# Kernel optimization log

Hardware: AMD Instinct MI355X
Metric: run time of the kernel (lower is better)

The kernel has to match this reference:

```python
import jax, jax.numpy as jnp
import numpy as np

S, H = 8192, 2048

def setup_inputs() -> dict:
    key = jax.random.key(0)
    k1, k2, k3 = jax.random.split(key, 3)
    hidden = jax.random.normal(k1, (1, H), dtype=jnp.float32)
    encoder_outputs = jax.random.normal(k2, (S, 1, H), dtype=jnp.float32)
    W = jax.random.normal(k3, (H, H), dtype=jnp.float32) * (1.0 / np.sqrt(H))
    b = jnp.zeros((H,), dtype=jnp.float32)
    return {"hidden": hidden, "encoder_outputs": encoder_outputs, "W": W, "b": b}

def reference(hidden, encoder_outputs, W, b):
    # hidden: [1, H] -> [H]; encoder_outputs: [S, 1, H] -> [S, H]
    h = hidden[0]                      # [H]
    enc = encoder_outputs[:, 0, :]     # [S, H]
    # method='general': energy_i = h . (W @ enc_i + b)
    proj = jnp.einsum('sh,kh->sk', enc, W) + b   # [S, H] (Linear: x @ W.T + b)
    energies = proj @ h                          # [S]
    attn = jax.nn.softmax(energies, axis=0)      # softmax over seq dim
    return attn[None, None, :]                   # [1, 1, S]
```

## Files before the change

### kernel.cpp

```cpp
#include <hip/hip_runtime.h>


#define Hdim 2048
#define Sdim 8192
#define PCHUNKS 128
#define PROWS 16

__global__ void k1_partial(const float* __restrict__ W, const float* __restrict__ hid,
                           float* __restrict__ part) {
    int t = threadIdx.x;
    int colBase = blockIdx.x * 1024 + t * 4;
    int k0 = blockIdx.y * PROWS;
    float4 acc = {0.f, 0.f, 0.f, 0.f};
#pragma unroll
    for (int i = 0; i < PROWS; ++i) {
        int k = k0 + i;
        float hk = hid[k];
        float4 w = *reinterpret_cast<const float4*>(W + (size_t)k * Hdim + colBase);
        acc.x += w.x * hk;
        acc.y += w.y * hk;
        acc.z += w.z * hk;
        acc.w += w.w * hk;
    }
    *reinterpret_cast<float4*>(part + (size_t)blockIdx.y * Hdim + colBase) = acc;
}

__global__ void k1b_reduce(const float* __restrict__ part, float* __restrict__ v) {
    __shared__ float red[256];
    int t = threadIdx.x;
    int col = blockIdx.x * 64 + (t & 63);
    int j0 = (t >> 6) * 32;
    float s = 0.f;
#pragma unroll
    for (int j = 0; j < 32; ++j) s += part[(size_t)(j0 + j) * Hdim + col];
    red[t] = s;
    __syncthreads();
    if (t < 64) v[col] = red[t] + red[64 + t] + red[128 + t] + red[192 + t];
}

__global__ void k2_energies(const float* __restrict__ enc, const float* __restrict__ v,
                            float* __restrict__ e) {
    int t = threadIdx.x;
    int lane = t & 63;
    int s = blockIdx.x * 4 + (t >> 6);
    const float* row = enc + (size_t)s * Hdim;
    float acc = 0.f;
#pragma unroll
    for (int i = 0; i < 8; ++i) {
        int idx = i * 256 + lane * 4;
        float4 a = *reinterpret_cast<const float4*>(row + idx);
        float4 w = *reinterpret_cast<const float4*>(v + idx);
        acc += a.x * w.x + a.y * w.y + a.z * w.z + a.w * w.w;
    }
#pragma unroll
    for (int off = 32; off > 0; off >>= 1) acc += __shfl_xor(acc, off, 64);
    if (lane == 0) e[s] = acc;
}

__global__ void k3_softmax(const float* __restrict__ e, float* __restrict__ out) {
    __shared__ float red[16];
    __shared__ float bcast;
    int t = threadIdx.x;
    int lane = t & 63, wid = t >> 6;
    float4 a = *reinterpret_cast<const float4*>(e + t * 8);
    float4 bq = *reinterpret_cast<const float4*>(e + t * 8 + 4);
    float vals[8] = {a.x, a.y, a.z, a.w, bq.x, bq.y, bq.z, bq.w};
    float m = vals[0];
#pragma unroll
    for (int i = 1; i < 8; ++i) m = fmaxf(m, vals[i]);
#pragma unroll
    for (int off = 32; off > 0; off >>= 1) m = fmaxf(m, __shfl_xor(m, off, 64));
    if (lane == 0) red[wid] = m;
    __syncthreads();
    if (wid == 0) {
        float mm = (lane < 16) ? red[lane] : -1e30f;
#pragma unroll
        for (int off = 8; off > 0; off >>= 1) mm = fmaxf(mm, __shfl_xor(mm, off, 64));
        if (lane == 0) bcast = mm;
    }
    __syncthreads();
    m = bcast;
    float ex[8];
    float s = 0.f;
#pragma unroll
    for (int i = 0; i < 8; ++i) {
        ex[i] = __expf(vals[i] - m);
        s += ex[i];
    }
#pragma unroll
    for (int off = 32; off > 0; off >>= 1) s += __shfl_xor(s, off, 64);
    __syncthreads();
    if (lane == 0) red[wid] = s;
    __syncthreads();
    if (wid == 0) {
        float ss = (lane < 16) ? red[lane] : 0.f;
#pragma unroll
        for (int off = 8; off > 0; off >>= 1) ss += __shfl_xor(ss, off, 64);
        if (lane == 0) bcast = ss;
    }
    __syncthreads();
    float inv = 1.0f / bcast;
    float4 o1 = {ex[0] * inv, ex[1] * inv, ex[2] * inv, ex[3] * inv};
    float4 o2 = {ex[4] * inv, ex[5] * inv, ex[6] * inv, ex[7] * inv};
    *reinterpret_cast<float4*>(out + t * 8) = o1;
    *reinterpret_cast<float4*>(out + t * 8 + 4) = o2;
}

extern "C" void kernel_launch(void* const* d_in, const int* in_sizes, int n_in,
                              void* d_out, int out_size, void* d_ws, size_t ws_size,
                              hipStream_t stream) {
    const float* hid = (const float*)d_in[0];
    const float* enc = (const float*)d_in[1];
    const float* W   = (const float*)d_in[2];
    float* out = (float*)d_out;
    float* ws = (float*)d_ws;

    float* part = ws;
    float* v    = part + PCHUNKS * Hdim;
    float* e    = v + Hdim;

    k1_partial<<<dim3(2, PCHUNKS), 256, 0, stream>>>(W, hid, part);
    k1b_reduce<<<32, 256, 0, stream>>>(part, v);
    k2_energies<<<Sdim / 4, 256, 0, stream>>>(enc, v, e);
    k3_softmax<<<1, 1024, 0, stream>>>(e, out);
}
```

Measured before the change: 26.52 us.

## Fuse W^T·h partial sums and reduction into one block-local kernel

Result: faster. 23.63 us (-10.9%).

```diff
diff --git a/kernel.cpp b/kernel.cpp
--- a/kernel.cpp
+++ b/kernel.cpp
@@ -3,39 +3,40 @@
 
 #define Hdim 2048
 #define Sdim 8192
-#define PCHUNKS 128
-#define PROWS 16
 
-__global__ void k1_partial(const float* __restrict__ W, const float* __restrict__ hid,
-                           float* __restrict__ part) {
+typedef float vfloat4 __attribute__((ext_vector_type(4)));
+
+__global__ void kv_matvec(const float* __restrict__ W, const float* __restrict__ hid,
+                          float* __restrict__ v) {
+    int b = blockIdx.x;
+    int c0 = (b & 7) * 256 + (b >> 3) * 8;
     int t = threadIdx.x;
-    int colBase = blockIdx.x * 1024 + t * 4;
-    int k0 = blockIdx.y * PROWS;
+    int cp = (t & 1) * 4;
+    int rl = t >> 1;
     float4 acc = {0.f, 0.f, 0.f, 0.f};
 #pragma unroll
-    for (int i = 0; i < PROWS; ++i) {
-        int k = k0 + i;
+    for (int i = 0; i < 8; ++i) {
+        int k = rl + 256 * i;
         float hk = hid[k];
-        float4 w = *reinterpret_cast<const float4*>(W + (size_t)k * Hdim + colBase);
+        float4 w = *reinterpret_cast<const float4*>(W + (size_t)k * Hdim + c0 + cp);
         acc.x += w.x * hk;
         acc.y += w.y * hk;
         acc.z += w.z * hk;
         acc.w += w.w * hk;
     }
-    *reinterpret_cast<float4*>(part + (size_t)blockIdx.y * Hdim + colBase) = acc;
-}
-
-__global__ void k1b_reduce(const float* __restrict__ part, float* __restrict__ v) {
-    __shared__ float red[256];
-    int t = threadIdx.x;
-    int col = blockIdx.x * 64 + (t & 63);
-    int j0 = (t >> 6) * 32;
-    float s = 0.f;
-#pragma unroll
-    for (int j = 0; j < 32; ++j) s += part[(size_t)(j0 + j) * Hdim + col];
-    red[t] = s;
+    __shared__ float4 red[512];
+    red[t] = acc;
     __syncthreads();
-    if (t < 64) v[col] = red[t] + red[64 + t] + red[128 + t] + red[192 + t];
+    for (int s = 128; s > 0; s >>= 1) {
+        if (rl < s) {
+            float4 o = red[t + 2 * s];
+            float4 m = red[t];
+            m.x += o.x; m.y += o.y; m.z += o.z; m.w += o.w;
+            red[t] = m;
+        }
+        __syncthreads();
+    }
+    if (t < 2) *reinterpret_cast<float4*>(v + c0 + t * 4) = red[t];
 }
 
 __global__ void k2_energies(const float* __restrict__ enc, const float* __restrict__ v,
@@ -48,7 +49,7 @@
 #pragma unroll
     for (int i = 0; i < 8; ++i) {
         int idx = i * 256 + lane * 4;
-        float4 a = *reinterpret_cast<const float4*>(row + idx);
+        vfloat4 a = __builtin_nontemporal_load(reinterpret_cast<const vfloat4*>(row + idx));
         float4 w = *reinterpret_cast<const float4*>(v + idx);
         acc += a.x * w.x + a.y * w.y + a.z * w.z + a.w * w.w;
     }
@@ -115,12 +116,10 @@
     float* out = (float*)d_out;
     float* ws = (float*)d_ws;
 
-    float* part = ws;
-    float* v    = part + PCHUNKS * Hdim;
-    float* e    = v + Hdim;
+    float* v = ws;
+    float* e = v + Hdim;
 
-    k1_partial<<<dim3(2, PCHUNKS), 256, 0, stream>>>(W, hid, part);
-    k1b_reduce<<<32, 256, 0, stream>>>(part, v);
+    kv_matvec<<<256, 512, 0, stream>>>(W, hid, v);
     k2_energies<<<Sdim / 4, 256, 0, stream>>>(enc, v, e);
     k3_softmax<<<1, 1024, 0, stream>>>(e, out);
 }
```
